# Optimization experiments

Measured on AMD Instinct MI355X. Metric: run time of the kernel, lower is better.

The kernel has to match this reference:

```python
import jax, jax.numpy as jnp
import numpy as np

B, T, N, H = 16, 12, 1000, 128
NL = 2  # num_layers
EPS = 1e-5


def setup_inputs() -> dict:
    key = jax.random.key(0)
    ks = jax.random.split(key, 16)
    rn = lambda k, s, sc=0.05: jax.random.normal(k, s, jnp.float32) * sc
    return {
        "inputs": jax.random.normal(ks[0], (B, T, N), jnp.float32),
        "adj": jax.random.uniform(ks[1], (N, N), dtype=jnp.float32),
        # per-layer graph-conv params (stacked over NL layers)
        "gc1_w": rn(ks[2], (NL, H + 1, 2 * H)),
        "gc1_b": jnp.ones((NL, 2 * H), jnp.float32),   # bias=1.0 in torch init
        "gc2_w": rn(ks[3], (NL, H + 1, H)),
        "gc2_b": jnp.zeros((NL, H), jnp.float32),
        "ln_g": jnp.ones((NL, H), jnp.float32),
        "ln_b": jnp.zeros((NL, H), jnp.float32),
        "res_w": rn(ks[4], (H,)),   # Linear(1,H) weight squeezed
        "res_b": rn(ks[5], (H,)),
        # GRU tail (unidirectional, 1 layer)
        "gru_wih": rn(ks[6], (3 * H, H)),
        "gru_whh": rn(ks[7], (3 * H, H)),
        "gru_bih": rn(ks[8], (3 * H,)),
        "gru_bhh": rn(ks[9], (3 * H,)),
        "proj_w": rn(ks[10], (H, H)),
        "proj_b": rn(ks[11], (H,)),
        # output MLP
        "out_w1": rn(ks[12], (256, H)),
        "out_b1": rn(ks[13], (256,)),
        "out_w2": rn(ks[14], (H, 256)),
        "out_b2": rn(ks[15], (H,)),
    }


def _laplacian(adj):
    a = jax.nn.softmax(adj, axis=-1)
    m = a + jnp.eye(N, dtype=adj.dtype)           # A + I
    d = m.sum(axis=1)
    dis = jnp.where(d > 0, d ** -0.5, 0.0)
    # matrix.matmul(D^-1/2).T.matmul(D^-1/2)
    return (m * dis[None, :]).T * dis[None, :]


def _gconv(L, x, h, w, b):
    # x: [B,N], h: [B,N,H], concat: [B,N,H+1]
    concat = jnp.concatenate([x[..., None], h], axis=2)
    ac = jnp.einsum("mn,bnk->bmk", L, concat)     # Laplacian graph conv
    return ac @ w + b                              # [B,N,out_dim]


def _cell(L, x, h, w1, b1, w2, b2):
    gates = jax.nn.sigmoid(_gconv(L, x, h, w1, b1))       # [B,N,2H]
    # torch chunks the FLAT [B, N*2H] tensor: split is across nodes!
    flat = gates.reshape(gates.shape[0], N * 2 * H)
    r = flat[:, : N * H].reshape(-1, N, H)
    u = flat[:, N * H :].reshape(-1, N, H)
    c = jnp.tanh(_gconv(L, x, r * h, w2, b2))
    return u * h + (1.0 - u) * c


def _layernorm(x, g, b):
    mu = x.mean(-1, keepdims=True)
    var = jnp.mean((x - mu) ** 2, axis=-1, keepdims=True)
    return (x - mu) * jax.lax.rsqrt(var + EPS) * g + b


def _gru_last(xs, h0, wih, whh, bih, bhh):
    # xs: [T, BN, H]
    def step(h, x):
        gi = x @ wih.T + bih
        gh = h @ whh.T + bhh
        ir, iz, inn = jnp.split(gi, 3, axis=-1)
        hr, hz, hn = jnp.split(gh, 3, axis=-1)
        r = jax.nn.sigmoid(ir + hr)
        z = jax.nn.sigmoid(iz + hz)
        n = jnp.tanh(inn + r * hn)
        return (1.0 - z) * n + z * h, None
    h_last, _ = jax.lax.scan(step, h0, xs)
    return h_last


def reference(inputs, adj, gc1_w, gc1_b, gc2_w, gc2_b, ln_g, ln_b, res_w, res_b,
              gru_wih, gru_whh, gru_bih, gru_bhh, proj_w, proj_b,
              out_w1, out_b1, out_w2, out_b2):
    L = _laplacian(adj)

    def step(hs, x_t):
        x = x_t
        residual = x_t
        new_hs = []
        out = None
        for i in range(NL):
            h = _cell(L, x, hs[i], gc1_w[i], gc1_b[i], gc2_w[i], gc2_b[i])
            new_hs.append(h)
            res = residual[..., None] * res_w + res_b   # Linear(1,H)
            out = _layernorm(h + res, ln_g[i], ln_b[i])  # dropout = identity (eval)
            x = out.mean(axis=2)
            residual = x
        return tuple(new_hs), out

    h0 = tuple(jnp.zeros((B, N, H), jnp.float32) for _ in range(NL))
    xs = jnp.swapaxes(inputs, 0, 1)                 # [T,B,N]
    _, outs = jax.lax.scan(step, h0, xs)            # [T,B,N,H]

    # GRU tail over time, batched across B*N node-sequences
    rnn_xs = jnp.transpose(outs, (0, 1, 2, 3)).reshape(T, B * N, H)
    h_last = _gru_last(rnn_xs, jnp.zeros((B * N, H), jnp.float32),
                       gru_wih, gru_whh, gru_bih, gru_bhh)
    last = h_last @ proj_w.T + proj_b
    o = last.reshape(B, N, H)
    o = jax.nn.relu(o @ out_w1.T + out_b1) @ out_w2.T + out_b2
    return o
```

## Files before the change

### kernel.cpp

```cpp
#include <hip/hip_runtime.h>
#include <math.h>

#define BB 16
#define TT 12
#define NN 1000
#define HH 128
#define CC 129
#define NROW 16000
#define GR 160
#define KP 1024
#define CP2 160
#define SPS 168

#define BUFSZ    22528
#define OFF_SGT  10752
#define OFF_SO   31232
#define OFF_SHB  39936
#define OFF_SCAL 67584
#define OFF_SST  70144
#define SMEMB    72192

typedef __attribute__((ext_vector_type(4))) float f32x4;
typedef __attribute__((ext_vector_type(8))) __bf16 bf16x8;

#define MFMA16(A, B, C) __builtin_amdgcn_mfma_f32_16x16x32_bf16((A), (B), (C), 0, 0, 0)

__device__ __forceinline__ float sigmoidf_(float x) { return 1.0f / (1.0f + expf(-x)); }

__global__ void k_softmax(const float* __restrict__ adj, float* __restrict__ a) {
    int i = blockIdx.x;
    int t = threadIdx.x;
    __shared__ float red[256];
    float m = -1e30f;
    for (int j = t; j < NN; j += 256) m = fmaxf(m, adj[i * NN + j]);
    red[t] = m; __syncthreads();
    for (int s = 128; s > 0; s >>= 1) { if (t < s) red[t] = fmaxf(red[t], red[t + s]); __syncthreads(); }
    m = red[0]; __syncthreads();
    float sum = 0.f;
    for (int j = t; j < NN; j += 256) sum += expf(adj[i * NN + j] - m);
    red[t] = sum; __syncthreads();
    for (int s = 128; s > 0; s >>= 1) { if (t < s) red[t] += red[t + s]; __syncthreads(); }
    float inv = 1.0f / red[0];
    for (int j = t; j < NN; j += 256) a[i * NN + j] = expf(adj[i * NN + j] - m) * inv;
}

__global__ __launch_bounds__(256) void k_build_Lt(const float* __restrict__ a, __bf16* __restrict__ Lb) {
    __shared__ float s[64][65];
    int bi = blockIdx.x * 64;
    int bj = blockIdx.y * 64;
    int t = threadIdx.x;
    for (int q = t; q < 64 * 64; q += 256) {
        int r = q >> 6, c = q & 63;
        int jj = bj + r, ii = bi + c;
        s[r][c] = (jj < NN && ii < NN) ? a[jj * NN + ii] : 0.f;
    }
    __syncthreads();
    for (int q = t; q < 64 * 64; q += 256) {
        int r = q >> 6, c = q & 63;
        int ii = bi + r, jj = bj + c;
        if (ii < NN && jj < NN)
            Lb[(size_t)ii * KP + jj] = (__bf16)(0.5f * (s[c][r] + (ii == jj ? 1.0f : 0.0f)));
    }
}

__global__ void k_prep(const float* __restrict__ wih, const float* __restrict__ whh,
                       const float* __restrict__ proj_w, const float* __restrict__ ow1,
                       const float* __restrict__ ow2, const float* __restrict__ gc1_w,
                       const float* __restrict__ gc2_w,
                       __bf16* __restrict__ WihB, __bf16* __restrict__ WhhB,
                       __bf16* __restrict__ projB, __bf16* __restrict__ w1B,
                       __bf16* __restrict__ w2B, __bf16* __restrict__ W1t,
                       __bf16* __restrict__ W2t) {
    int idx = blockIdx.x * 256 + threadIdx.x;
    if (idx < 49152) { WihB[idx] = (__bf16)wih[idx]; return; }
    idx -= 49152;
    if (idx < 49152) { WhhB[idx] = (__bf16)whh[idx]; return; }
    idx -= 49152;
    if (idx < 16384) { projB[idx] = (__bf16)proj_w[idx]; return; }
    idx -= 16384;
    if (idx < 32768) { w1B[idx] = (__bf16)ow1[idx]; return; }
    idx -= 32768;
    if (idx < 32768) { w2B[idx] = (__bf16)ow2[idx]; return; }
    idx -= 32768;
    if (idx < 2 * 256 * CP2) {
        int l = idx / (256 * CP2); int r = idx % (256 * CP2); int o = r / CP2, c = r % CP2;
        W1t[idx] = (c < CC) ? (__bf16)gc1_w[((size_t)l * CC + c) * 256 + o] : (__bf16)0.f;
        return;
    }
    idx -= 2 * 256 * CP2;
    if (idx < 2 * 128 * CP2) {
        int l = idx / (128 * CP2); int r = idx % (128 * CP2); int o = r / CP2, c = r % CP2;
        W2t[idx] = (c < CC) ? (__bf16)gc2_w[((size_t)l * CC + c) * 128 + o] : (__bf16)0.f;
    }
}

__global__ void k_prep_x(const float* __restrict__ inp, __bf16* __restrict__ G0) {
    int idx = blockIdx.x * 256 + threadIdx.x;
    if (idx >= BB * 1024) return;
    int b = idx >> 10, k = idx & 1023;
    G0[(size_t)b * GR * KP + k] = (k < NN) ? (__bf16)inp[(size_t)b * TT * NN + k] : (__bf16)0.f;
}

#define GL16(SRC, DSTOFF)                                                            \
    __builtin_amdgcn_global_load_lds(                                                \
        (const __attribute__((address_space(1))) unsigned int*)(SRC),                \
        (__attribute__((address_space(3))) unsigned int*)(smem + (DSTOFF)), 16, 0, 0)

template<int MODE, int STORE>
__global__ __launch_bounds__(512) void k_fused(
    const __bf16* __restrict__ Lb, const __bf16* __restrict__ Gf,
    const __bf16* __restrict__ Wt, const float* __restrict__ bias,
    __bf16* __restrict__ GB, __bf16* __restrict__ u, __bf16* __restrict__ h,
    const float* __restrict__ x_in, int xstride,
    const float* __restrict__ res_w, const float* __restrict__ res_b,
    const float* __restrict__ ln_g, const float* __restrict__ ln_b,
    float* __restrict__ x_out, __bf16* __restrict__ Gnext,
    __bf16* __restrict__ GhSelf,
    __bf16* __restrict__ Hb,
    const __bf16* __restrict__ WihB, const __bf16* __restrict__ WhhB,
    const float* __restrict__ bih, const float* __restrict__ bhh,
    const float* __restrict__ inp, __bf16* __restrict__ xnextG, int tnext)
{
    __shared__ __align__(16) char smem[SMEMB];
    __bf16* sP   = (__bf16*)smem;
    __bf16* sGT  = (__bf16*)(smem + OFF_SGT);
    __bf16* sT   = (__bf16*)(smem + OFF_SGT);
    __bf16* sO   = (__bf16*)(smem + OFF_SO);
    float*  sScal= (float*)(smem + OFF_SCAL);
    float*  sSt  = (float*)(smem + OFF_SST);

    int tid = threadIdx.x;
    int wg = blockIdx.x;
    int b = wg & 15;
    int m0 = (wg >> 4) * 32;
    int wave = tid >> 6, lane = tid & 63;
    int lr = lane & 15, lk = lane >> 4;
    int wm = wave >> 2;
    int wcg = wave & 3;
    int cgbase = (wcg == 0) ? 0 : (wcg * 2 + 1) * 16;
    int NC = (wcg == 0) ? 3 : 2;

    if (MODE == 0) {
        if (tid < 256) sScal[tid] = bias[tid];
    } else if (tid < 128) {
        sScal[tid] = bias[tid];
        sScal[128 + tid] = res_w[tid];
        sScal[256 + tid] = res_b[tid];
        sScal[384 + tid] = ln_g[tid];
        sScal[512 + tid] = ln_b[tid];
    }

    size_t srowOff = (size_t)b * GR * KP;
    int rIn = lane >> 3;
    int cswz = ((lane & 7) ^ rIn) * 8;

    int nld = (wave < 6) ? 3 : 2;
    const __bf16* psrc[3];
    int pdst[3];
#pragma unroll
    for (int q = 0; q < 3; q++) {
        int c = wave + q * 8;
        if (c < 22) {
            psrc[q] = (c < 4)
                ? Lb + (size_t)(m0 + c * 8 + rIn) * KP + cswz
                : Gf + srowOff + (size_t)((c - 4) * 8 + rIn) * KP + cswz;
            pdst[q] = c * 1024;
        } else { psrc[q] = nullptr; pdst[q] = 0; }
    }

#define STAGE(BUF, IT) {                                                     \
    _Pragma("unroll")                                                        \
    for (int q = 0; q < 3; q++)                                              \
        if (wave + q * 8 < 22)                                               \
            GL16(psrc[q] + (IT) * 64, (BUF) * BUFSZ + pdst[q]); }

    f32x4 acc[3];
#pragma unroll
    for (int j = 0; j < 3; j++) acc[j] = (f32x4){0.f, 0.f, 0.f, 0.f};

    STAGE(0, 0);
    __syncthreads();
    STAGE(1, 1);
    int bc = 0;
    for (int it = 0; it < 16; ++it) {
        if (it == 15) asm volatile("s_waitcnt vmcnt(0)" ::: "memory");
        else if (nld == 3) asm volatile("s_waitcnt vmcnt(3)" ::: "memory");
        else               asm volatile("s_waitcnt vmcnt(2)" ::: "memory");
        __builtin_amdgcn_s_barrier();
        __builtin_amdgcn_sched_barrier(0);
        const char* bp = smem + bc * BUFSZ;
#pragma unroll
        for (int ks = 0; ks < 2; ks++) {
            int kb = (ks * 64 + lk * 16) ^ ((lr & 7) << 4);
            int chA = wm * 2 + (lr >> 3);
            bf16x8 af = *(const bf16x8*)(bp + chA * 1024 + (lr & 7) * 128 + kb);
#pragma unroll
            for (int cf = 0; cf < 3; cf++) {
                if (cf < NC) {
                    int chB = 4 + (cgbase >> 3) + cf * 2 + (lr >> 3);
                    bf16x8 bfr = *(const bf16x8*)(bp + chB * 1024 + (lr & 7) * 128 + kb);
                    acc[cf] = MFMA16(af, bfr, acc[cf]);
                }
            }
        }
        if (it < 14) { int bs = (it + 2) % 3; STAGE(bs, it + 2); }
        bc = (bc == 2) ? 0 : bc + 1;
    }
    __syncthreads();
#undef STAGE

#pragma unroll
    for (int cf = 0; cf < 3; cf++) {
        if (cf < NC) {
#pragma unroll
            for (int i = 0; i < 4; i++)
                sP[(wm * 16 + lk * 4 + i) * SPS + cgbase + cf * 16 + lr] = (__bf16)acc[cf][i];
        }
    }
    for (int q = tid; q < 32 * 16; q += 512) sP[(q >> 4) * SPS + 144 + (q & 15)] = (__bf16)0.f;
    __syncthreads();

    constexpr int NOF = (MODE == 0) ? 2 : 1;
    int o0 = wave * NOF * 16;
    int j = o0 + lr;
    f32x4 accs[2][NOF];
#pragma unroll
    for (int i = 0; i < 2; i++)
#pragma unroll
        for (int jj = 0; jj < NOF; jj++) accs[i][jj] = (f32x4){0.f, 0.f, 0.f, 0.f};
#pragma unroll
    for (int kk2 = 0; kk2 < CP2; kk2 += 32) {
        bf16x8 pa[2];
#pragma unroll
        for (int mf2 = 0; mf2 < 2; mf2++)
            pa[mf2] = *(const bf16x8*)&sP[(mf2 * 16 + lr) * SPS + kk2 + lk * 8];
#pragma unroll
        for (int of = 0; of < NOF; of++) {
            bf16x8 wb = *(const bf16x8*)&Wt[(size_t)(o0 + of * 16 + lr) * CP2 + kk2 + lk * 8];
#pragma unroll
            for (int mf2 = 0; mf2 < 2; mf2++)
                accs[mf2][of] = MFMA16(pa[mf2], wb, accs[mf2][of]);
        }
    }

    if (MODE == 0) {
        if (tid < 4)
            *(bf16x8*)&GB[srowOff + m0 + tid * 8] = *(const bf16x8*)&Gf[srowOff + m0 + tid * 8];
        bool clean = (m0 + 32 <= 500);
        if (clean) {
#pragma unroll
            for (int of = 0; of < NOF; of++) {
                int o = o0 + of * 16 + lr;
                float bv = sScal[o];
#pragma unroll
                for (int mf2 = 0; mf2 < 2; mf2++)
#pragma unroll
                    for (int i = 0; i < 4; i++)
                        sGT[o * 40 + mf2 * 16 + lk * 4 + i] = (__bf16)sigmoidf_(accs[mf2][of][i] + bv);
            }
            __syncthreads();
            for (int q = tid; q < 128 * 8; q += 512) {
                int jj = q >> 3;
                int rnc = (q & 7) * 4;
                size_t gidx = srowOff + (size_t)(1 + jj) * KP + 2 * m0 + rnc * 2;
                bf16x8 hv = *(const bf16x8*)&Gf[gidx];
                bf16x8 rv;
#pragma unroll
                for (int e = 0; e < 8; e++) {
                    int rnl = rnc + (e >> 1);
                    int hi = e & 1;
                    float g = (float)sGT[(hi * 128 + jj) * 40 + rnl];
                    rv[e] = (__bf16)(g * (float)hv[e]);
                }
                *(bf16x8*)&GB[gidx] = rv;
            }
        } else {
#pragma unroll
            for (int of = 0; of < NOF; of++) {
                int o = o0 + of * 16 + lr;
                int jo = o & 127, hi = o >> 7;
                float bv = sScal[o];
#pragma unroll
                for (int mf2 = 0; mf2 < 2; mf2++)
#pragma unroll
                    for (int i = 0; i < 4; i++) {
                        int m = m0 + mf2 * 16 + lk * 4 + i;
                        if (m >= NN) continue;
                        float g = sigmoidf_(accs[mf2][of][i] + bv);
                        if (m < 500) {
                            size_t gi = srowOff + (size_t)(1 + jo) * KP + 2 * m + hi;
                            GB[gi] = (__bf16)(g * (float)Gf[gi]);
                        } else {
                            u[((size_t)b * NN + 2 * (m - 500) + hi) * HH + jo] = (__bf16)g;
                        }
                    }
            }
        }
    } else {
        float hnv[2][4];
        float mu_[2][4], rs_[2][4];
        float xs_[2][4];
        {
            float s_[2][4], ss_[2][4];
#pragma unroll
            for (int a = 0; a < 2; a++)
#pragma unroll
                for (int i = 0; i < 4; i++) { s_[a][i] = 0.f; ss_[a][i] = 0.f; }
            float b2v = sScal[j], rwv = sScal[128 + j], rbv = sScal[256 + j];
#pragma unroll
            for (int mf2 = 0; mf2 < 2; mf2++) {
#pragma unroll
                for (int i = 0; i < 4; i++) {
                    int m = m0 + mf2 * 16 + lk * 4 + i;
                    int msafe = (m < NN) ? m : (NN - 1);
                    size_t ri = ((size_t)b * NN + msafe) * HH + j;
                    float cv = tanhf(accs[mf2][0][i] + b2v);
                    float uu = (float)u[ri];
                    float hv = (float)h[ri];
                    float hn = uu * hv + (1.f - uu) * cv;
                    if (m < NN) h[ri] = (__bf16)hn;
                    hnv[mf2][i] = hn;
                    float xv = (m < NN) ? x_in[(size_t)b * xstride + m] : 0.f;
                    float y = hn + xv * rwv + rbv;
                    accs[mf2][0][i] = y;
                    s_[mf2][i] += y; ss_[mf2][i] += y * y;
                }
            }
#pragma unroll
            for (int msk = 1; msk < 16; msk <<= 1)
#pragma unroll
                for (int a = 0; a < 2; a++)
#pragma unroll
                    for (int i = 0; i < 4; i++) {
                        s_[a][i] += __shfl_xor(s_[a][i], msk);
                        ss_[a][i] += __shfl_xor(ss_[a][i], msk);
                    }
            if (lr == 0) {
#pragma unroll
                for (int a = 0; a < 2; a++)
#pragma unroll
                    for (int i = 0; i < 4; i++) {
                        int ml = a * 16 + lk * 4 + i;
                        sSt[wave * 32 + ml] = s_[a][i];
                        sSt[256 + wave * 32 + ml] = ss_[a][i];
                    }
            }
        }
        __syncthreads();
        {
#pragma unroll
            for (int a = 0; a < 2; a++)
#pragma unroll
                for (int i = 0; i < 4; i++) {
                    int ml = a * 16 + lk * 4 + i;
                    float S = 0.f, SS = 0.f;
#pragma unroll
                    for (int w = 0; w < 8; w++) { S += sSt[w * 32 + ml]; SS += sSt[256 + w * 32 + ml]; }
                    float mu = S * (1.f / 128.f);
                    float var = SS * (1.f / 128.f) - mu * mu;
                    mu_[a][i] = mu;
                    rs_[a][i] = rsqrtf(var + 1e-5f);
                }
            float lg = sScal[384 + j], lb2 = sScal[512 + j];
#pragma unroll
            for (int mf2 = 0; mf2 < 2; mf2++)
#pragma unroll
                for (int i = 0; i < 4; i++) {
                    float ov = (accs[mf2][0][i] - mu_[mf2][i]) * rs_[mf2][i] * lg + lb2;
                    accs[mf2][0][i] = ov;
                    xs_[mf2][i] = ov;
                }
#pragma unroll
            for (int msk = 1; msk < 16; msk <<= 1)
#pragma unroll
                for (int a = 0; a < 2; a++)
#pragma unroll
                    for (int i = 0; i < 4; i++) xs_[a][i] += __shfl_xor(xs_[a][i], msk);
        }
        __syncthreads();
        if (lr == 0) {
#pragma unroll
            for (int a = 0; a < 2; a++)
#pragma unroll
                for (int i = 0; i < 4; i++)
                    sSt[wave * 32 + a * 16 + lk * 4 + i] = xs_[a][i];
        }
        __syncthreads();
        if (wave == 0 && lr == 0) {
#pragma unroll
            for (int a = 0; a < 2; a++)
#pragma unroll
                for (int i = 0; i < 4; i++) {
                    int ml = a * 16 + lk * 4 + i;
                    int m = m0 + ml;
                    if (m < NN) {
                        float S = 0.f;
#pragma unroll
                        for (int w = 0; w < 8; w++) S += sSt[w * 32 + ml];
                        float xv = S * (1.f / 128.f);
                        if (x_out) x_out[(size_t)b * NN + m] = xv;
                        if (Gnext) Gnext[(size_t)b * GR * KP + m] = (__bf16)xv;
                    }
                }
        }
        {
#pragma unroll
            for (int mf2 = 0; mf2 < 2; mf2++)
#pragma unroll
                for (int i = 0; i < 4; i++)
                    sT[j * 40 + mf2 * 16 + lk * 4 + i] = (__bf16)hnv[mf2][i];
            if (STORE) {
#pragma unroll
                for (int mf2 = 0; mf2 < 2; mf2++)
#pragma unroll
                    for (int i = 0; i < 4; i++)
                        sO[(mf2 * 16 + lk * 4 + i) * 136 + j] = (__bf16)accs[mf2][0][i];
            }
        }
        if (STORE) {
            int row = tid >> 4, c8 = (tid & 15) * 8;
            int m = m0 + row;
            size_t hrow = (size_t)b * NN + ((m < NN) ? m : (NN - 1));
            *(bf16x8*)(smem + OFF_SHB + (row * 136 + c8) * 2) =
                *(const bf16x8*)&Hb[hrow * HH + c8];
        }
        __syncthreads();
        {
            int q = tid;
            int jj = q >> 2, mc = (q & 3) * 8;
            if (m0 + mc < NN)
                *(bf16x8*)&GhSelf[srowOff + (size_t)(1 + jj) * KP + m0 + mc] =
                    *(const bf16x8*)&sT[jj * 40 + mc];
        }
        if (STORE) {
            {
                float br  = bih[j] + bhh[j];
                float bz  = bih[128 + j] + bhh[128 + j];
                float bni = bih[256 + j], bnh = bhh[256 + j];
                const __bf16* wir = WihB + (size_t)j * HH;
                const __bf16* whr = WhhB + (size_t)j * HH;
                const __bf16* wiz = WihB + (size_t)(128 + j) * HH;
                const __bf16* whz = WhhB + (size_t)(128 + j) * HH;
                const __bf16* win = WihB + (size_t)(256 + j) * HH;
                const __bf16* whn = WhhB + (size_t)(256 + j) * HH;
#pragma unroll
                for (int mf = 0; mf < 2; mf++) {
                    f32x4 gr = (f32x4){0.f,0.f,0.f,0.f}, gz = gr, gni = gr, gnh = gr;
#pragma unroll
                    for (int kk = 0; kk < 128; kk += 32) {
                        bf16x8 xa = *(const bf16x8*)&sO[(mf * 16 + lr) * 136 + kk + lk * 8];
                        bf16x8 ha = *(const bf16x8*)(smem + OFF_SHB + ((mf * 16 + lr) * 136 + kk + lk * 8) * 2);
                        gr  = MFMA16(xa, *(const bf16x8*)(wir + kk + lk * 8), gr);
                        gr  = MFMA16(ha, *(const bf16x8*)(whr + kk + lk * 8), gr);
                        gz  = MFMA16(xa, *(const bf16x8*)(wiz + kk + lk * 8), gz);
                        gz  = MFMA16(ha, *(const bf16x8*)(whz + kk + lk * 8), gz);
                        gni = MFMA16(xa, *(const bf16x8*)(win + kk + lk * 8), gni);
                        gnh = MFMA16(ha, *(const bf16x8*)(whn + kk + lk * 8), gnh);
                    }
#pragma unroll
                    for (int i = 0; i < 4; i++) {
                        int m = m0 + mf * 16 + lk * 4 + i;
                        if (m >= NN) continue;
                        size_t ri = ((size_t)b * NN + m) * HH + j;
                        float hv = (float)*(const __bf16*)(smem + OFF_SHB +
                                      ((mf * 16 + lk * 4 + i) * 136 + j) * 2);
                        float rg = sigmoidf_(gr[i] + br);
                        float zg = sigmoidf_(gz[i] + bz);
                        float ng = tanhf(gni[i] + bni + rg * (gnh[i] + bnh));
                        float hp = (1.f - zg) * ng + zg * hv;
                        Hb[ri] = (__bf16)hp;
                    }
                }
            }
            if (tid < 32 && tnext < TT) {
                int n = m0 + tid;
                if (n < NN)
                    xnextG[srowOff + n] = (__bf16)inp[(size_t)b * TT * NN + tnext * NN + n];
            }
        }
    }
}
#undef GL16

__global__ __launch_bounds__(256) void k_head_mfma(const __bf16* __restrict__ Hb,
                                                   const __bf16* __restrict__ projB,
                                                   const float* __restrict__ pb,
                                                   const __bf16* __restrict__ w1B,
                                                   const float* __restrict__ b1,
                                                   const __bf16* __restrict__ w2B,
                                                   const float* __restrict__ b2,
                                                   float* __restrict__ out) {
    __shared__ __align__(16) __bf16 sH1[64 * 136];
    __shared__ __align__(16) __bf16 sH2[64 * 264];
    int tid = threadIdx.x;
    int r0 = blockIdx.x * 64;
    int wv = tid >> 6, lane = tid & 63;
    int lr = lane & 15, lk = lane >> 4;
    int arow = r0 + wv * 16 + lr;

    f32x4 a1[8];
#pragma unroll
    for (int i = 0; i < 8; i++) a1[i] = (f32x4){0.f, 0.f, 0.f, 0.f};
#pragma unroll
    for (int kk = 0; kk < 128; kk += 32) {
        bf16x8 xa = *(const bf16x8*)&Hb[(size_t)arow * HH + kk + lk * 8];
#pragma unroll
        for (int f = 0; f < 8; f++) {
            bf16x8 wb = *(const bf16x8*)&projB[(size_t)(f * 16 + lr) * HH + kk + lk * 8];
            a1[f] = MFMA16(xa, wb, a1[f]);
        }
    }
#pragma unroll
    for (int f = 0; f < 8; f++) {
        int j = f * 16 + lr;
        float bv = pb[j];
#pragma unroll
        for (int i = 0; i < 4; i++)
            sH1[(wv * 16 + lk * 4 + i) * 136 + j] = (__bf16)(a1[f][i] + bv);
    }
    __syncthreads();

    f32x4 a2[16];
#pragma unroll
    for (int i = 0; i < 16; i++) a2[i] = (f32x4){0.f, 0.f, 0.f, 0.f};
#pragma unroll
    for (int kk = 0; kk < 128; kk += 32) {
        bf16x8 pa = *(const bf16x8*)&sH1[(wv * 16 + lr) * 136 + kk + lk * 8];
#pragma unroll
        for (int f = 0; f < 16; f++) {
            bf16x8 wb = *(const bf16x8*)&w1B[(size_t)(f * 16 + lr) * HH + kk + lk * 8];
            a2[f] = MFMA16(pa, wb, a2[f]);
        }
    }
    __syncthreads();
#pragma unroll
    for (int f = 0; f < 16; f++) {
        int o = f * 16 + lr;
        float bv = b1[o];
#pragma unroll
        for (int i = 0; i < 4; i++)
            sH2[(wv * 16 + lk * 4 + i) * 264 + o] = (__bf16)fmaxf(a2[f][i] + bv, 0.f);
    }
    __syncthreads();

    f32x4 a3[8];
#pragma unroll
    for (int i = 0; i < 8; i++) a3[i] = (f32x4){0.f, 0.f, 0.f, 0.f};
#pragma unroll
    for (int kk = 0; kk < 256; kk += 32) {
        bf16x8 pa = *(const bf16x8*)&sH2[(wv * 16 + lr) * 264 + kk + lk * 8];
#pragma unroll
        for (int f = 0; f < 8; f++) {
            bf16x8 wb = *(const bf16x8*)&w2B[(size_t)(f * 16 + lr) * 256 + kk + lk * 8];
            a3[f] = MFMA16(pa, wb, a3[f]);
        }
    }
#pragma unroll
    for (int f = 0; f < 8; f++) {
        int j = f * 16 + lr;
        float bv = b2[j];
#pragma unroll
        for (int i = 0; i < 4; i++)
            out[(size_t)(r0 + wv * 16 + lk * 4 + i) * HH + j] = a3[f][i] + bv;
    }
}

extern "C" void kernel_launch(void* const* d_in, const int* in_sizes, int n_in,
                              void* d_out, int out_size, void* d_ws, size_t ws_size,
                              hipStream_t stream) {
    const float* inp    = (const float*)d_in[0];
    const float* adj    = (const float*)d_in[1];
    const float* gc1_w  = (const float*)d_in[2];
    const float* gc1_b  = (const float*)d_in[3];
    const float* gc2_w  = (const float*)d_in[4];
    const float* gc2_b  = (const float*)d_in[5];
    const float* ln_g   = (const float*)d_in[6];
    const float* ln_b   = (const float*)d_in[7];
    const float* res_w  = (const float*)d_in[8];
    const float* res_b  = (const float*)d_in[9];
    const float* wih    = (const float*)d_in[10];
    const float* whh    = (const float*)d_in[11];
    const float* bih    = (const float*)d_in[12];
    const float* bhh    = (const float*)d_in[13];
    const float* proj_w = (const float*)d_in[14];
    const float* proj_b = (const float*)d_in[15];
    const float* ow1    = (const float*)d_in[16];
    const float* ob1    = (const float*)d_in[17];
    const float* ow2    = (const float*)d_in[18];
    const float* ob2    = (const float*)d_in[19];
    float* out = (float*)d_out;

    char* ws = (char*)d_ws;
    size_t off = 0;
    __bf16* Lb     = (__bf16*)(ws + off); off += (size_t)KP * KP * 2;
    __bf16* Gfull0 = (__bf16*)(ws + off); off += (size_t)BB * GR * KP * 2;
    __bf16* Gfull1 = (__bf16*)(ws + off); off += (size_t)BB * GR * KP * 2;
    __bf16* GfullB = (__bf16*)(ws + off); off += (size_t)BB * GR * KP * 2;
    size_t zgrp1 = off;
    __bf16* h0  = (__bf16*)(ws + off); off += (size_t)NROW * HH * 2;
    __bf16* h1  = (__bf16*)(ws + off); off += (size_t)NROW * HH * 2;
    __bf16* Hb  = (__bf16*)(ws + off); off += (size_t)NROW * HH * 2;
    size_t zgrp2 = off;
    __bf16* u   = (__bf16*)(ws + off); off += (size_t)NROW * HH * 2;
    float* xB   = (float*)(ws + off);  off += NROW * 4;
    __bf16* W1t = (__bf16*)(ws + off); off += (size_t)2 * 256 * CP2 * 2;
    __bf16* W2t = (__bf16*)(ws + off); off += (size_t)2 * 128 * CP2 * 2;
    __bf16* WihB= (__bf16*)(ws + off); off += 49152 * 2;
    __bf16* WhhB= (__bf16*)(ws + off); off += 49152 * 2;
    __bf16* projB=(__bf16*)(ws + off); off += 16384 * 2;
    __bf16* w1B = (__bf16*)(ws + off); off += 32768 * 2;
    __bf16* w2B = (__bf16*)(ws + off); off += 32768 * 2;
    float* a_sm = (float*)u;

    hipMemsetAsync(Lb, 0, zgrp1, stream);
    hipMemsetAsync(h0, 0, zgrp2 - zgrp1, stream);

    k_softmax<<<NN, 256, 0, stream>>>(adj, a_sm);
    k_build_Lt<<<dim3(16, 16), 256, 0, stream>>>(a_sm, Lb);
    k_prep<<<1184, 256, 0, stream>>>(wih, whh, proj_w, ow1, ow2, gc1_w, gc2_w,
                                     WihB, WhhB, projB, w1B, w2B, W1t, W2t);
    k_prep_x<<<64, 256, 0, stream>>>(inp, Gfull0);

    for (int t = 0; t < TT; t++) {
        const float* xs0 = inp + (size_t)t * NN;
        k_fused<0, 0><<<512, 512, 0, stream>>>(Lb, Gfull0, W1t, gc1_b, GfullB, u,
            nullptr, nullptr, 0, nullptr, nullptr, nullptr, nullptr,
            nullptr, nullptr, nullptr,
            nullptr, nullptr, nullptr, nullptr, nullptr, nullptr, nullptr, 0);
        k_fused<1, 0><<<512, 512, 0, stream>>>(Lb, GfullB, W2t, gc2_b, nullptr, u, h0,
            xs0, TT * NN, res_w, res_b, ln_g, ln_b,
            xB, Gfull1, Gfull0,
            nullptr, nullptr, nullptr, nullptr, nullptr, nullptr, nullptr, 0);
        k_fused<0, 0><<<512, 512, 0, stream>>>(Lb, Gfull1, W1t + 256 * CP2, gc1_b + 256, GfullB, u,
            nullptr, nullptr, 0, nullptr, nullptr, nullptr, nullptr,
            nullptr, nullptr, nullptr,
            nullptr, nullptr, nullptr, nullptr, nullptr, nullptr, nullptr, 0);
        k_fused<1, 1><<<512, 512, 0, stream>>>(Lb, GfullB, W2t + 128 * CP2, gc2_b + 128, nullptr, u, h1,
            xB, NN, res_w, res_b, ln_g + 128, ln_b + 128,
            nullptr, nullptr, Gfull1,
            Hb, WihB, WhhB, bih, bhh, inp, Gfull0, t + 1);
    }
    k_head_mfma<<<250, 256, 0, stream>>>(Hb, projB, proj_b, w1B, ob1, w2B, ob2, out);
}
```

Measured before the change: 1.320 ms.

## Load Laplacian tile once into LDS and stream G operands from global to registers

Replaces the triple-buffered global_load_lds pipeline, which staged both the Laplacian rows and the G rows through LDS on every k-iteration, with a single up-front swizzled copy of the full 32x1024 Laplacian tile into LDS. The G (B operand) fragments are now loaded straight from global memory into registers with a two-stage register double buffer, and the per-iteration barriers go away. This cuts LDS traffic and synchronisation in the main loop, but relies on uncoalesced per-lane global loads of G and raises register pressure.

```diff
diff --git a/kernel.cpp b/kernel.cpp
--- a/kernel.cpp
+++ b/kernel.cpp
@@ -12,13 +12,12 @@
 #define CP2 160
 #define SPS 168
 
-#define BUFSZ    22528
 #define OFF_SGT  10752
 #define OFF_SO   31232
 #define OFF_SHB  39936
-#define OFF_SCAL 67584
-#define OFF_SST  70144
-#define SMEMB    72192
+#define OFF_SCAL 65536
+#define OFF_SST  68096
+#define SMEMB    70144
 
 typedef __attribute__((ext_vector_type(4))) float f32x4;
 typedef __attribute__((ext_vector_type(8))) __bf16 bf16x8;
@@ -101,11 +100,6 @@
     G0[(size_t)b * GR * KP + k] = (k < NN) ? (__bf16)inp[(size_t)b * TT * NN + k] : (__bf16)0.f;
 }
 
-#define GL16(SRC, DSTOFF)                                                            \
-    __builtin_amdgcn_global_load_lds(                                                \
-        (const __attribute__((address_space(1))) unsigned int*)(SRC),                \
-        (__attribute__((address_space(3))) unsigned int*)(smem + (DSTOFF)), 16, 0, 0)
-
 template<int MODE, int STORE>
 __global__ __launch_bounds__(512) void k_fused(
     const __bf16* __restrict__ Lb, const __bf16* __restrict__ Gf,
@@ -151,63 +145,58 @@
     }
 
     size_t srowOff = (size_t)b * GR * KP;
-    int rIn = lane >> 3;
-    int cswz = ((lane & 7) ^ rIn) * 8;
-
-    int nld = (wave < 6) ? 3 : 2;
-    const __bf16* psrc[3];
-    int pdst[3];
-#pragma unroll
-    for (int q = 0; q < 3; q++) {
-        int c = wave + q * 8;
-        if (c < 22) {
-            psrc[q] = (c < 4)
-                ? Lb + (size_t)(m0 + c * 8 + rIn) * KP + cswz
-                : Gf + srowOff + (size_t)((c - 4) * 8 + rIn) * KP + cswz;
-            pdst[q] = c * 1024;
-        } else { psrc[q] = nullptr; pdst[q] = 0; }
-    }
-
-#define STAGE(BUF, IT) {                                                     \
-    _Pragma("unroll")                                                        \
-    for (int q = 0; q < 3; q++)                                              \
-        if (wave + q * 8 < 22)                                               \
-            GL16(psrc[q] + (IT) * 64, (BUF) * BUFSZ + pdst[q]); }
+
+#pragma unroll
+    for (int p = 0; p < 8; ++p) {
+        int q = tid + p * 512;
+        int row = q >> 7, c16 = q & 127;
+        bf16x8 v = *(const bf16x8*)&Lb[(size_t)(m0 + row) * KP + c16 * 8];
+        *(bf16x8*)(smem + row * 2048 + ((c16 ^ (row & 7)) << 4)) = v;
+    }
+    __syncthreads();
 
     f32x4 acc[3];
 #pragma unroll
-    for (int j = 0; j < 3; j++) acc[j] = (f32x4){0.f, 0.f, 0.f, 0.f};
-
-    STAGE(0, 0);
+    for (int j3 = 0; j3 < 3; j3++) acc[j3] = (f32x4){0.f, 0.f, 0.f, 0.f};
+
+    const __bf16* gp[3];
+#pragma unroll
+    for (int cf = 0; cf < 3; cf++) {
+        int rc = (cf < NC) ? (cgbase + cf * 16 + lr) : cgbase;
+        gp[cf] = Gf + srowOff + (size_t)rc * KP + lk * 8;
+    }
+    int rowA = wm * 16 + lr;
+    const char* lbase = smem + rowA * 2048;
+    int rx = rowA & 7;
+
+    bf16x8 gA[2][3], gB[2][3];
+#define LDG(DST, IT) {                                                         \
+    _Pragma("unroll")                                                          \
+    for (int ks = 0; ks < 2; ks++)                                             \
+        _Pragma("unroll")                                                      \
+        for (int cf = 0; cf < 3; cf++)                                         \
+            if (cf < NC) DST[ks][cf] = *(const bf16x8*)(gp[cf] + (IT) * 64 + ks * 32); }
+#define CMP(SRC, IT) {                                                         \
+    _Pragma("unroll")                                                          \
+    for (int ks = 0; ks < 2; ks++) {                                           \
+        int c16 = (IT) * 8 + ks * 4 + lk;                                      \
+        bf16x8 af = *(const bf16x8*)(lbase + ((c16 ^ rx) << 4));               \
+        _Pragma("unroll")                                                      \
+        for (int cf = 0; cf < 3; cf++)                                         \
+            if (cf < NC) acc[cf] = MFMA16(af, SRC[ks][cf], acc[cf]);           \
+    } }
+
+    LDG(gA, 0);
+#pragma unroll
+    for (int it = 0; it < 16; it += 2) {
+        LDG(gB, it + 1);
+        CMP(gA, it);
+        if (it + 2 < 16) LDG(gA, it + 2);
+        CMP(gB, it + 1);
+    }
+#undef LDG
+#undef CMP
     __syncthreads();
-    STAGE(1, 1);
-    int bc = 0;
-    for (int it = 0; it < 16; ++it) {
-        if (it == 15) asm volatile("s_waitcnt vmcnt(0)" ::: "memory");
-        else if (nld == 3) asm volatile("s_waitcnt vmcnt(3)" ::: "memory");
-        else               asm volatile("s_waitcnt vmcnt(2)" ::: "memory");
-        __builtin_amdgcn_s_barrier();
-        __builtin_amdgcn_sched_barrier(0);
-        const char* bp = smem + bc * BUFSZ;
-#pragma unroll
-        for (int ks = 0; ks < 2; ks++) {
-            int kb = (ks * 64 + lk * 16) ^ ((lr & 7) << 4);
-            int chA = wm * 2 + (lr >> 3);
-            bf16x8 af = *(const bf16x8*)(bp + chA * 1024 + (lr & 7) * 128 + kb);
-#pragma unroll
-            for (int cf = 0; cf < 3; cf++) {
-                if (cf < NC) {
-                    int chB = 4 + (cgbase >> 3) + cf * 2 + (lr >> 3);
-                    bf16x8 bfr = *(const bf16x8*)(bp + chB * 1024 + (lr & 7) * 128 + kb);
-                    acc[cf] = MFMA16(af, bfr, acc[cf]);
-                }
-            }
-        }
-        if (it < 14) { int bs = (it + 2) % 3; STAGE(bs, it + 2); }
-        bc = (bc == 2) ? 0 : bc + 1;
-    }
-    __syncthreads();
-#undef STAGE
 
 #pragma unroll
     for (int cf = 0; cf < 3; cf++) {
@@ -480,7 +469,6 @@
         }
     }
 }
-#undef GL16
 
 __global__ __launch_bounds__(256) void k_head_mfma(const __bf16* __restrict__ Hb,
                                                    const __bf16* __restrict__ projB,
```

Result: slower. 2.459 ms (+86.3%).
